# Kernel optimization log

Measured on AMD Instinct MI355X. Metric: run time of the kernel, lower is better.

Reference implementation:

```python
import jax, jax.numpy as jnp
import numpy as np

N = 50000
E = 400000
IN_DIM = 256
H1, D1 = 4, 128   # gat1: heads=4, hidden=128, concat -> 512
H2, D2 = 1, 64    # gat2: heads=1, out=64, concat=False
NEG_SLOPE = 0.2


def setup_inputs() -> dict:
    key = jax.random.key(0)
    ks = jax.random.split(key, 12)
    x = jax.random.normal(ks[0], (N, IN_DIM), dtype=jnp.float32)
    edge_index = jax.random.randint(ks[1], (2, E), 0, N, dtype=jnp.int64)
    edge_attr = jax.random.normal(ks[2], (E,), dtype=jnp.float32)
    # Glorot-ish init for weights, zeros for biases (as in PyG GATConv)
    def glorot(k, shape):
        fan = shape[0] + shape[-1]
        return jax.random.normal(k, shape, dtype=jnp.float32) * jnp.sqrt(2.0 / fan)
    W1 = glorot(ks[3], (IN_DIM, H1 * D1))
    a1_src = glorot(ks[4], (H1, D1))
    a1_dst = glorot(ks[5], (H1, D1))
    b1 = jnp.zeros((H1 * D1,), dtype=jnp.float32)
    W2 = glorot(ks[6], (H1 * D1, H2 * D2))
    a2_src = glorot(ks[7], (H2, D2))
    a2_dst = glorot(ks[8], (H2, D2))
    b2 = jnp.zeros((D2,), dtype=jnp.float32)
    return {"x": x, "edge_index": edge_index, "edge_attr": edge_attr,
            "W1": W1, "a1_src": a1_src, "a1_dst": a1_dst, "b1": b1,
            "W2": W2, "a2_src": a2_src, "a2_dst": a2_dst, "b2": b2}


def _gat_layer(x, src, dst, W, a_s, a_d, b, heads, d, concat):
    n = x.shape[0]
    h = (x @ W).reshape(n, heads, d)                      # [N,H,D]
    alpha_s = jnp.einsum('nhd,hd->nh', h, a_s)            # [N,H]
    alpha_d = jnp.einsum('nhd,hd->nh', h, a_d)
    e = jax.nn.leaky_relu(alpha_s[src] + alpha_d[dst], NEG_SLOPE)  # [Etot,H]
    # segment softmax over incoming edges of each dst node
    emax = jax.ops.segment_max(e, dst, num_segments=n)
    ex = jnp.exp(e - emax[dst])
    denom = jax.ops.segment_sum(ex, dst, num_segments=n)
    alpha = ex / (denom[dst] + 1e-16)                     # [Etot,H]
    msg = h[src] * alpha[:, :, None]                      # [Etot,H,D]
    out = jax.ops.segment_sum(msg, dst, num_segments=n)   # [N,H,D]
    out = out.reshape(n, heads * d) if concat else out.mean(axis=1)
    return out + b


def reference(x, edge_index, edge_attr, W1, a1_src, a1_dst, b1,
              W2, a2_src, a2_dst, b2):
    # edge_attr is ignored (GATConv built without edge_dim)
    loop = jnp.arange(N, dtype=edge_index.dtype)          # PyG add_self_loops=True
    src = jnp.concatenate([edge_index[0], loop])
    dst = jnp.concatenate([edge_index[1], loop])
    h = _gat_layer(x, src, dst, W1, a1_src, a1_dst, b1, H1, D1, True)
    h = jax.nn.elu(h)
    out = _gat_layer(h, src, dst, W2, a2_src, a2_dst, b2, H2, D2, False)
    return out
```

## Files before the change

### kernel.cpp

```cpp
#include <hip/hip_runtime.h>
#include <cstdint>

typedef unsigned short u16;
typedef short bf16x8_t __attribute__((ext_vector_type(8)));
typedef float f32x4_t __attribute__((ext_vector_type(4)));

#define DEVFN __device__ __forceinline__

DEVFN u16 f2bf(float f) {
  unsigned u = __builtin_bit_cast(unsigned, f);
  u = (u + 0x7fffu + ((u >> 16) & 1u)) >> 16;
  return (u16)u;
}
DEVFN float bf2f(u16 s) {
  unsigned u = ((unsigned)s) << 16;
  return __builtin_bit_cast(float, u);
}
DEVFN unsigned pk2bf(float a, float b) {
  return (unsigned)f2bf(a) | ((unsigned)f2bf(b) << 16);
}

DEVFN void gload_lds16(const u16* g, u16* l) {
  __builtin_amdgcn_global_load_lds(
      (const __attribute__((address_space(1))) void*)g,
      (__attribute__((address_space(3))) void*)l, 16, 0, 0);
}

__global__ void prep_kernel(const float* __restrict__ W1, const float* __restrict__ W2,
                            const float* __restrict__ a1s, const float* __restrict__ a1d,
                            const int* __restrict__ edst,
                            u16* __restrict__ w1t, u16* __restrict__ w2t,
                            float* __restrict__ ws1, float* __restrict__ wd1,
                            int* __restrict__ cnt, int e) {
  int b = blockIdx.x;
  if (b < 512) {
    int idx = b * 256 + threadIdx.x;
    int k = idx >> 9, m = idx & 511;
    w1t[m * 256 + k] = f2bf(W1[idx]);
  } else if (b < 640) {
    int idx = (b - 512) * 256 + threadIdx.x;
    int k = idx >> 6, m = idx & 63;
    w2t[m * 512 + k] = f2bf(W2[idx]);
  } else if (b < 648) {
    int b2 = b - 640;
    int h = b2 >> 1;
    int isD = b2 & 1;
    const float* av = (isD ? a1d : a1s) + h * 128;
    int k = threadIdx.x;
    float sum = 0.f;
#pragma unroll 8
    for (int d = 0; d < 128; ++d)
      sum = fmaf(W1[k * 512 + h * 128 + d], av[d], sum);
    (isD ? wd1 : ws1)[h * 256 + k] = sum;
  } else {
    int i = (b - 648) * 256 + threadIdx.x;
    if (i < e) atomicAdd(&cnt[edst[i]], 1);
  }
}

__global__ __launch_bounds__(256) void conv_alpha_kernel(
    const float* __restrict__ x, const float* __restrict__ ws1, const float* __restrict__ wd1,
    u16* __restrict__ xb, float* __restrict__ as1, float* __restrict__ ad1, int n)
{
  int node = (blockIdx.x * 256 + threadIdx.x) >> 6;
  int lane = threadIdx.x & 63;
  if (node >= n) return;
  float4 xv = *reinterpret_cast<const float4*>(x + (size_t)node * 256 + lane * 4);
  uint2 pk;
  pk.x = pk2bf(xv.x, xv.y);
  pk.y = pk2bf(xv.z, xv.w);
  *reinterpret_cast<uint2*>(xb + (size_t)node * 256 + lane * 4) = pk;

  float p[8];
#pragma unroll
  for (int v = 0; v < 8; ++v) {
    const float* wv = (v < 4 ? ws1 : wd1) + (v & 3) * 256 + lane * 4;
    float4 w4 = *reinterpret_cast<const float4*>(wv);
    p[v] = xv.x * w4.x + xv.y * w4.y + xv.z * w4.z + xv.w * w4.w;
  }
#pragma unroll
  for (int d = 1; d < 64; d <<= 1) {
#pragma unroll
    for (int v = 0; v < 8; ++v) p[v] += __shfl_xor(p[v], d, 64);
  }
  if (lane == 0) {
    *reinterpret_cast<float4*>(as1 + (size_t)node * 4) = make_float4(p[0], p[1], p[2], p[3]);
    *reinterpret_cast<float4*>(ad1 + (size_t)node * 4) = make_float4(p[4], p[5], p[6], p[7]);
  }
}

DEVFN int block_scan_256(int v, int tid, int* wsum) {
#pragma unroll
  for (int d = 1; d < 64; d <<= 1) {
    int u = __shfl_up(v, d, 64);
    if ((tid & 63) >= d) v += u;
  }
  if ((tid & 63) == 63) wsum[tid >> 6] = v;
  __syncthreads();
  int add = 0;
#pragma unroll
  for (int w = 0; w < 4; ++w) add += (w < (tid >> 6)) ? wsum[w] : 0;
  __syncthreads();
  return v + add;
}

__global__ __launch_bounds__(256) void scan_a_kernel(const int* __restrict__ cnt, int* __restrict__ bsum, int n) {
  __shared__ int ws4[4];
  int i = blockIdx.x * 256 + threadIdx.x;
  int v = (i < n) ? cnt[i] + 1 : 0;
  int incl = block_scan_256(v, threadIdx.x, ws4);
  if (threadIdx.x == 255) bsum[blockIdx.x] = incl;
}

__global__ __launch_bounds__(256) void scan_c_kernel(
    const int* __restrict__ cnt, const int* __restrict__ bsum,
    int* __restrict__ rowoff, int* __restrict__ cursor, int n)
{
  __shared__ int ws4[4];
  __shared__ int ws4b[4];
  __shared__ int base_sh;
  int pre = 0;
  for (int w = threadIdx.x; w < blockIdx.x; w += 256) pre += bsum[w];
#pragma unroll
  for (int d = 1; d < 64; d <<= 1) pre += __shfl_xor(pre, d, 64);
  if ((threadIdx.x & 63) == 0) ws4b[threadIdx.x >> 6] = pre;
  __syncthreads();
  if (threadIdx.x == 0) base_sh = ws4b[0] + ws4b[1] + ws4b[2] + ws4b[3];
  int i = blockIdx.x * 256 + threadIdx.x;
  int v = (i < n) ? cnt[i] + 1 : 0;
  int incl = block_scan_256(v, threadIdx.x, ws4);
  int off = base_sh + incl - v;
  if (i < n) {
    rowoff[i] = off;
    cursor[i] = off;
    if (i == n - 1) rowoff[n] = off + v;
  }
}

__global__ void scatter_kernel(const int* __restrict__ srcs, const int* __restrict__ dsts,
                               int* __restrict__ cursor, int* __restrict__ csr, int e, int n) {
  int i = blockIdx.x * 256 + threadIdx.x;
  if (i >= e + n) return;
  int s, d;
  if (i < e) { s = srcs[i]; d = dsts[i]; }
  else       { s = i - e; d = s; }
  int pos = atomicAdd(&cursor[d], 1);
  csr[pos] = s;
}

__global__ __launch_bounds__(256) void aggx_kernel(
    const u16* __restrict__ xb, const float* __restrict__ as1,
    const float* __restrict__ ad1, const int* __restrict__ rowoff,
    const int* __restrict__ csr, u16* __restrict__ aggx, size_t plane, int n)
{
  int node = (blockIdx.x * 256 + threadIdx.x) >> 6;
  int lane = threadIdx.x & 63;
  if (node >= n) return;
  int e0 = rowoff[node], e1 = rowoff[node + 1];
  float4 adv = *reinterpret_cast<const float4*>(ad1 + (size_t)node * 4);
  const unsigned dimb = (unsigned)lane * 4;

  float acc[4][4];
#pragma unroll
  for (int h = 0; h < 4; ++h)
#pragma unroll
    for (int d = 0; d < 4; ++d) acc[h][d] = 0.f;
  float den[4] = {0.f, 0.f, 0.f, 0.f};

  for (int e = e0; e < e1; ++e) {
    unsigned s = (unsigned)csr[e];
    float4 a4 = *reinterpret_cast<const float4*>(as1 + ((size_t)s << 2));
    float ex[4];
    {
      float t0 = a4.x + adv.x, t1 = a4.y + adv.y, t2 = a4.z + adv.z, t3 = a4.w + adv.w;
      ex[0] = __expf(fmaxf(t0, 0.2f * t0));
      ex[1] = __expf(fmaxf(t1, 0.2f * t1));
      ex[2] = __expf(fmaxf(t2, 0.2f * t2));
      ex[3] = __expf(fmaxf(t3, 0.2f * t3));
    }
#pragma unroll
    for (int h = 0; h < 4; ++h) den[h] += ex[h];
    uint2 xv = *reinterpret_cast<const uint2*>(xb + (((size_t)s << 8) + dimb));
    float xf[4];
    xf[0] = bf2f((u16)(xv.x & 0xffffu));
    xf[1] = bf2f((u16)(xv.x >> 16));
    xf[2] = bf2f((u16)(xv.y & 0xffffu));
    xf[3] = bf2f((u16)(xv.y >> 16));
#pragma unroll
    for (int h = 0; h < 4; ++h)
#pragma unroll
      for (int d = 0; d < 4; ++d) acc[h][d] = fmaf(ex[h], xf[d], acc[h][d]);
  }

#pragma unroll
  for (int h = 0; h < 4; ++h) {
    float inv = 1.f / (den[h] + 1e-16f);
    uint2 o;
    o.x = pk2bf(acc[h][0] * inv, acc[h][1] * inv);
    o.y = pk2bf(acc[h][2] * inv, acc[h][3] * inv);
    *reinterpret_cast<uint2*>(aggx + (size_t)h * plane + ((size_t)node << 8) + dimb) = o;
  }
}

template<int BM, int BN, int WROWS, int K, int BK, int NP>
__global__ __launch_bounds__(256) void gemm1_kernel(
    const u16* __restrict__ Aall, const u16* __restrict__ BT,
    const float* __restrict__ b1, u16* __restrict__ C, int M, size_t plane)
{
  constexpr int WM = BM / WROWS;
  constexpr int MF = WM / 16;
  constexpr int NF = BN / 16;
  constexpr int KK = BK / 32;
  static_assert(BK == 64, "swizzle derived for 128B rows");
  __shared__ __align__(16) u16 sA[BM][BK];
  __shared__ __align__(16) u16 sB[BN][BK];

  const int tid = threadIdx.x;
  const int lane = tid & 63;
  const int wr = tid >> 6;

  const int bid = blockIdx.x;
  const int xcd = bid & 7;
  const int rest = bid >> 3;
  const int p = rest & (NP - 1);
  const int rb = rest / NP;
  const int r = rb * 8 + xcd;
  const int NRB = (M + BM - 1) / BM;
  if (r >= NRB) return;
  const int brow = r * BM;
  const int bcol = p * BN;
  const u16* A = Aall + (size_t)p * plane;

  f32x4_t acc[MF][NF];
#pragma unroll
  for (int i = 0; i < MF; ++i)
#pragma unroll
    for (int j = 0; j < NF; ++j) acc[i][j] = f32x4_t{0.f, 0.f, 0.f, 0.f};

  const int rsel = lane & 15;
  const int kgrp = (lane >> 4) * 8;
  const int rx = (rsel & 7) * 8;

#pragma unroll
  for (int k0 = 0; k0 < K; k0 += BK) {
    constexpr int RA = BM * BK / 2048;
    bf16x8_t av[RA];
#pragma unroll
    for (int c = 0; c < RA; ++c) {
      int t = c * 256 + tid;
      int row = t >> 3;
      int gr = brow + row; gr = gr < M ? gr : M - 1;
      av[c] = *reinterpret_cast<const bf16x8_t*>(A + (size_t)gr * K + k0 + (t & 7) * 8);
    }
#pragma unroll
    for (int c = 0; c < RA; ++c) {
      int t = c * 256 + tid;
      int row = t >> 3;
      int slot = (t & 7) ^ (row & 7);
      *reinterpret_cast<bf16x8_t*>(&sA[0][0] + row * BK + slot * 8) = av[c];
    }
    constexpr int RB = BN * BK / 2048;
#pragma unroll
    for (int c = 0; c < RB; ++c) {
      int t = c * 256 + tid;
      int row = t >> 3;
      int col = ((t & 7) ^ (row & 7)) * 8;
      gload_lds16(BT + (size_t)(bcol + row) * K + k0 + col, &sB[0][0] + t * 8);
    }
    __syncthreads();
#pragma unroll
    for (int kk = 0; kk < KK; ++kk) {
      const int cswz = (kk * 32 + kgrp) ^ rx;
      bf16x8_t af[MF], bfr[NF];
#pragma unroll
      for (int i = 0; i < MF; ++i) {
        int row = wr * WM + i * 16 + rsel;
        af[i] = *reinterpret_cast<const bf16x8_t*>(&sA[0][0] + row * BK + cswz);
      }
#pragma unroll
      for (int j = 0; j < NF; ++j) {
        int row = j * 16 + rsel;
        bfr[j] = *reinterpret_cast<const bf16x8_t*>(&sB[0][0] + row * BK + cswz);
      }
#pragma unroll
      for (int i = 0; i < MF; ++i)
#pragma unroll
        for (int j = 0; j < NF; ++j)
          acc[i][j] = __builtin_amdgcn_mfma_f32_16x16x32_bf16(af[i], bfr[j], acc[i][j], 0, 0, 0);
    }
    __syncthreads();
  }

  const int crow0 = (lane >> 4) * 4;
  const int ccol = lane & 15;
#pragma unroll
  for (int i = 0; i < MF; ++i)
#pragma unroll
    for (int j = 0; j < NF; ++j)
#pragma unroll
      for (int rr = 0; rr < 4; ++rr) {
        int gr = brow + wr * WM + i * 16 + crow0 + rr;
        int gc = bcol + j * 16 + ccol;
        if (gr < M) {
          float v = acc[i][j][rr] + b1[gc];
          v = v > 0.f ? v : (__expf(v) - 1.0f);
          C[(size_t)gr * 512 + gc] = f2bf(v);
        }
      }
}

template<int BM, int BN, int WROWS, int K, int BK, int H, int DH>
__global__ __launch_bounds__(256) void gemm_alpha_kernel(
    const u16* __restrict__ A, const u16* __restrict__ BT, u16* __restrict__ C,
    const float* __restrict__ a_s, const float* __restrict__ a_d,
    float* __restrict__ as_out, float* __restrict__ ad_out, int M, int N)
{
  static_assert(BN == DH, "alpha store ownership");
  static_assert(BK == 64, "swizzle derived for 128B rows");
  constexpr int WM = BM / WROWS;
  constexpr int MF = WM / 16;
  constexpr int NF = BN / 16;
  constexpr int KK = BK / 32;
  __shared__ __align__(16) u16 sA[BM][BK];
  __shared__ __align__(16) u16 sB[BN][BK];

  const int tid = threadIdx.x;
  const int lane = tid & 63;
  const int wr = tid >> 6;
  const int brow = blockIdx.x * BM;
  const int bcol = blockIdx.y * BN;

  f32x4_t acc[MF][NF];
#pragma unroll
  for (int i = 0; i < MF; ++i)
#pragma unroll
    for (int j = 0; j < NF; ++j) acc[i][j] = f32x4_t{0.f, 0.f, 0.f, 0.f};

  const int rsel = lane & 15;
  const int kgrp = (lane >> 4) * 8;
  const int rx = (rsel & 7) * 8;

#pragma unroll
  for (int k0 = 0; k0 < K; k0 += BK) {
    constexpr int RA = BM * BK / 2048;
#pragma unroll
    for (int c = 0; c < RA; ++c) {
      int t = c * 256 + tid;
      int row = t >> 3;
      int col = ((t & 7) ^ (row & 7)) * 8;
      int gr = brow + row; gr = gr < M ? gr : M - 1;
      gload_lds16(A + (size_t)gr * K + k0 + col, &sA[0][0] + t * 8);
    }
    constexpr int RB = BN * BK / 2048;
#pragma unroll
    for (int c = 0; c < RB; ++c) {
      int t = c * 256 + tid;
      int row = t >> 3;
      int col = ((t & 7) ^ (row & 7)) * 8;
      gload_lds16(BT + (size_t)(bcol + row) * K + k0 + col, &sB[0][0] + t * 8);
    }
    __syncthreads();
#pragma unroll
    for (int kk = 0; kk < KK; ++kk) {
      const int cswz = (kk * 32 + kgrp) ^ rx;
      bf16x8_t af[MF], bfr[NF];
#pragma unroll
      for (int i = 0; i < MF; ++i) {
        int row = wr * WM + i * 16 + rsel;
        af[i] = *reinterpret_cast<const bf16x8_t*>(&sA[0][0] + row * BK + cswz);
      }
#pragma unroll
      for (int j = 0; j < NF; ++j) {
        int row = j * 16 + rsel;
        bfr[j] = *reinterpret_cast<const bf16x8_t*>(&sB[0][0] + row * BK + cswz);
      }
#pragma unroll
      for (int i = 0; i < MF; ++i)
#pragma unroll
        for (int j = 0; j < NF; ++j)
          acc[i][j] = __builtin_amdgcn_mfma_f32_16x16x32_bf16(af[i], bfr[j], acc[i][j], 0, 0, 0);
    }
    __syncthreads();
  }

  const int crow0 = (lane >> 4) * 4;
  const int ccol = lane & 15;

#pragma unroll
  for (int i = 0; i < MF; ++i)
#pragma unroll
    for (int j = 0; j < NF; ++j)
#pragma unroll
      for (int rr = 0; rr < 4; ++rr) {
        int gr = brow + wr * WM + i * 16 + crow0 + rr;
        int gc = bcol + j * 16 + ccol;
        if (gr < M) C[(size_t)gr * N + gc] = f2bf(acc[i][j][rr]);
      }

  const int head = bcol / DH;
  float asv[NF], adv[NF];
#pragma unroll
  for (int j = 0; j < NF; ++j) {
    int gc = bcol + j * 16 + ccol;
    asv[j] = a_s[gc];
    adv[j] = a_d[gc];
  }
#pragma unroll
  for (int i = 0; i < MF; ++i) {
#pragma unroll
    for (int rr = 0; rr < 4; ++rr) {
      float ps = 0.f, pd = 0.f;
#pragma unroll
      for (int j = 0; j < NF; ++j) {
        float v = acc[i][j][rr];
        ps = fmaf(v, asv[j], ps);
        pd = fmaf(v, adv[j], pd);
      }
#pragma unroll
      for (int d = 1; d < 16; d <<= 1) {
        ps += __shfl_xor(ps, d, 64);
        pd += __shfl_xor(pd, d, 64);
      }
      if ((lane & 15) == 0) {
        int gr = brow + wr * WM + i * 16 + crow0 + rr;
        if (gr < M) {
          as_out[(size_t)gr * H + head] = ps;
          ad_out[(size_t)gr * H + head] = pd;
        }
      }
    }
  }
}

__global__ __launch_bounds__(256) void agg2_kernel(
    const u16* __restrict__ h2, const float* __restrict__ as2,
    const float* __restrict__ ad2, const int* __restrict__ rowoff,
    const int* __restrict__ csr, const float* __restrict__ b2,
    float* __restrict__ out, int n)
{
  int node = (blockIdx.x * 256 + threadIdx.x) >> 5;
  int l32 = threadIdx.x & 31;
  if (node >= n) return;
  int e0 = rowoff[node], e1 = rowoff[node + 1];
  float advn = ad2[node];

  float acc0 = 0.f, acc1 = 0.f, den = 0.f;
  for (int e = e0; e < e1; ++e) {
    unsigned s = (unsigned)csr[e];
    float t = as2[s] + advn;
    float l = fmaxf(t, 0.2f * t);
    float ex = __expf(l);
    den += ex;
    unsigned hv = *reinterpret_cast<const unsigned*>(h2 + (s << 6) + l32 * 2);
    acc0 = fmaf(ex, bf2f((u16)(hv & 0xffffu)), acc0);
    acc1 = fmaf(ex, bf2f((u16)(hv >> 16)), acc1);
  }
  float inv = 1.f / (den + 1e-16f);
  float2 o;
  o.x = acc0 * inv + b2[l32 * 2];
  o.y = acc1 * inv + b2[l32 * 2 + 1];
  *reinterpret_cast<float2*>(out + (((size_t)node) << 6) + l32 * 2) = o;
}

extern "C" void kernel_launch(void* const* d_in, const int* in_sizes, int n_in,
                              void* d_out, int out_size, void* d_ws, size_t ws_size,
                              hipStream_t stream) {
  const float* x   = (const float*)d_in[0];
  const int*   ei  = (const int*)d_in[1];
  const float* W1  = (const float*)d_in[3];
  const float* a1s = (const float*)d_in[4];
  const float* a1d = (const float*)d_in[5];
  const float* b1  = (const float*)d_in[6];
  const float* W2  = (const float*)d_in[7];
  const float* a2s = (const float*)d_in[8];
  const float* a2d = (const float*)d_in[9];
  const float* b2  = (const float*)d_in[10];
  float* out = (float*)d_out;

  const int IN_DIM = 256, H1D1 = 512, D2 = 64;
  const int N = in_sizes[0] / IN_DIM;
  const int E = in_sizes[1] / 2;

  char* ws = (char*)d_ws;
  size_t off = 0;
  auto alloc = [&](size_t bytes) -> void* {
    void* p = ws + off;
    off += (bytes + 255) & ~(size_t)255;
    return p;
  };
  u16*  w1t    = (u16*)alloc((size_t)H1D1 * IN_DIM * 2);
  u16*  w2t    = (u16*)alloc((size_t)D2 * H1D1 * 2);
  float* ws1   = (float*)alloc(4 * 256 * 4);
  float* wd1   = (float*)alloc(4 * 256 * 4);
  u16*  xb     = (u16*)alloc((size_t)N * IN_DIM * 2);
  float* as1   = (float*)alloc((size_t)N * 4 * 4);
  float* ad1   = (float*)alloc((size_t)N * 4 * 4);
  int*  cnt    = (int*)alloc((size_t)N * 4);
  int*  cursor = (int*)alloc((size_t)N * 4);
  int*  rowoff = (int*)alloc((size_t)(N + 1) * 4);
  int*  bsum   = (int*)alloc(256 * 4);
  int*  csr    = (int*)alloc((size_t)(E + N) * 4);
  size_t plane = (size_t)N * IN_DIM;
  u16*  aggx   = (u16*)alloc(4 * plane * 2);
  u16*  h1o    = (u16*)alloc((size_t)N * H1D1 * 2);
  (void)n_in; (void)out_size; (void)ws_size;

  u16*   h2b = xb;
  float* as2 = (float*)(xb + (size_t)N * D2);
  float* ad2 = as2 + N;

  const int* esrc = ei;
  const int* edst = ei + E;

  (void)hipMemsetAsync(cnt, 0, (size_t)N * 4, stream);

  int eb = (E + 255) / 256;
  prep_kernel<<<648 + eb, 256, 0, stream>>>(W1, W2, a1s, a1d, edst, w1t, w2t, ws1, wd1, cnt, E);

  conv_alpha_kernel<<<(N + 3) / 4, 256, 0, stream>>>(x, ws1, wd1, xb, as1, ad1, N);

  int nsb = (N + 255) / 256;
  scan_a_kernel<<<nsb, 256, 0, stream>>>(cnt, bsum, N);
  scan_c_kernel<<<nsb, 256, 0, stream>>>(cnt, bsum, rowoff, cursor, N);
  scatter_kernel<<<(E + N + 255) / 256, 256, 0, stream>>>(esrc, edst, cursor, csr, E, N);

  aggx_kernel<<<(N + 3) / 4, 256, 0, stream>>>(xb, as1, ad1, rowoff, csr, aggx, plane, N);

  const int NRB = (N + 127) / 128;
  const int g1 = ((NRB + 7) / 8) * 8 * 4;
  gemm1_kernel<128, 128, 4, 256, 64, 4><<<g1, 256, 0, stream>>>(aggx, w1t, b1, h1o, N, plane);

  dim3 g2((N + 63) / 64, 1);
  gemm_alpha_kernel<64, 64, 4, 512, 64, 1, 64><<<g2, 256, 0, stream>>>(
      h1o, w2t, h2b, a2s, a2d, as2, ad2, N, D2);

  agg2_kernel<<<((size_t)N * 32 + 255) / 256, 256, 0, stream>>>(h2b, as2, ad2, rowoff, csr, b2, out, N);
}
```

Before: 255.5 us.

## Software-pipeline GEMM k-loop with register-prefetched A and double-buffered B tiles

Both GEMM kernels now prefetch the next K-slice during the MFMA work on the current one. A is loaded into registers and B goes into a second LDS buffer. The intent is to hide global-load latency behind compute instead of stalling at each barrier. gemm_alpha switches A from direct LDS loads to register staging. The change adds LDS and register pressure, and there is a possible hazard: sA is overwritten after only one barrier per step, so a write could race with the previous step's reads.

```diff
diff --git a/kernel.cpp b/kernel.cpp
--- a/kernel.cpp
+++ b/kernel.cpp
@@ -211,9 +211,10 @@
   constexpr int MF = WM / 16;
   constexpr int NF = BN / 16;
   constexpr int KK = BK / 32;
+  constexpr int NSTEP = K / BK;
   static_assert(BK == 64, "swizzle derived for 128B rows");
   __shared__ __align__(16) u16 sA[BM][BK];
-  __shared__ __align__(16) u16 sB[BN][BK];
+  __shared__ __align__(16) u16 sB[2][BN][BK];
 
   const int tid = threadIdx.x;
   const int lane = tid & 63;
@@ -241,17 +242,27 @@
   const int kgrp = (lane >> 4) * 8;
   const int rx = (rsel & 7) * 8;
 
-#pragma unroll
-  for (int k0 = 0; k0 < K; k0 += BK) {
-    constexpr int RA = BM * BK / 2048;
-    bf16x8_t av[RA];
-#pragma unroll
-    for (int c = 0; c < RA; ++c) {
-      int t = c * 256 + tid;
-      int row = t >> 3;
-      int gr = brow + row; gr = gr < M ? gr : M - 1;
-      av[c] = *reinterpret_cast<const bf16x8_t*>(A + (size_t)gr * K + k0 + (t & 7) * 8);
-    }
+  constexpr int RA = BM * BK / 2048;
+  constexpr int RBn = BN * BK / 2048;
+  bf16x8_t av[RA];
+
+#pragma unroll
+  for (int c = 0; c < RA; ++c) {
+    int t = c * 256 + tid;
+    int row = t >> 3;
+    int gr = brow + row; gr = gr < M ? gr : M - 1;
+    av[c] = *reinterpret_cast<const bf16x8_t*>(A + (size_t)gr * K + (t & 7) * 8);
+  }
+#pragma unroll
+  for (int c = 0; c < RBn; ++c) {
+    int t = c * 256 + tid;
+    int row = t >> 3;
+    int col = ((t & 7) ^ (row & 7)) * 8;
+    gload_lds16(BT + (size_t)(bcol + row) * K + col, &sB[0][0][0] + t * 8);
+  }
+
+#pragma unroll
+  for (int k = 0; k < NSTEP; ++k) {
 #pragma unroll
     for (int c = 0; c < RA; ++c) {
       int t = c * 256 + tid;
@@ -259,15 +270,24 @@
       int slot = (t & 7) ^ (row & 7);
       *reinterpret_cast<bf16x8_t*>(&sA[0][0] + row * BK + slot * 8) = av[c];
     }
-    constexpr int RB = BN * BK / 2048;
-#pragma unroll
-    for (int c = 0; c < RB; ++c) {
-      int t = c * 256 + tid;
-      int row = t >> 3;
-      int col = ((t & 7) ^ (row & 7)) * 8;
-      gload_lds16(BT + (size_t)(bcol + row) * K + k0 + col, &sB[0][0] + t * 8);
-    }
     __syncthreads();
+    if (k + 1 < NSTEP) {
+      const int k0n = (k + 1) * BK;
+#pragma unroll
+      for (int c = 0; c < RA; ++c) {
+        int t = c * 256 + tid;
+        int row = t >> 3;
+        int gr = brow + row; gr = gr < M ? gr : M - 1;
+        av[c] = *reinterpret_cast<const bf16x8_t*>(A + (size_t)gr * K + k0n + (t & 7) * 8);
+      }
+#pragma unroll
+      for (int c = 0; c < RBn; ++c) {
+        int t = c * 256 + tid;
+        int row = t >> 3;
+        int col = ((t & 7) ^ (row & 7)) * 8;
+        gload_lds16(BT + (size_t)(bcol + row) * K + k0n + col, &sB[(k + 1) & 1][0][0] + t * 8);
+      }
+    }
 #pragma unroll
     for (int kk = 0; kk < KK; ++kk) {
       const int cswz = (kk * 32 + kgrp) ^ rx;
@@ -280,7 +300,7 @@
 #pragma unroll
       for (int j = 0; j < NF; ++j) {
         int row = j * 16 + rsel;
-        bfr[j] = *reinterpret_cast<const bf16x8_t*>(&sB[0][0] + row * BK + cswz);
+        bfr[j] = *reinterpret_cast<const bf16x8_t*>(&sB[k & 1][0][0] + row * BK + cswz);
       }
 #pragma unroll
       for (int i = 0; i < MF; ++i)
@@ -321,8 +341,9 @@
   constexpr int MF = WM / 16;
   constexpr int NF = BN / 16;
   constexpr int KK = BK / 32;
+  constexpr int NSTEP = K / BK;
   __shared__ __align__(16) u16 sA[BM][BK];
-  __shared__ __align__(16) u16 sB[BN][BK];
+  __shared__ __align__(16) u16 sB[2][BN][BK];
 
   const int tid = threadIdx.x;
   const int lane = tid & 63;
@@ -340,26 +361,52 @@
   const int kgrp = (lane >> 4) * 8;
   const int rx = (rsel & 7) * 8;
 
-#pragma unroll
-  for (int k0 = 0; k0 < K; k0 += BK) {
-    constexpr int RA = BM * BK / 2048;
+  constexpr int RA = BM * BK / 2048;
+  constexpr int RBn = BN * BK / 2048;
+  bf16x8_t av[RA];
+
+#pragma unroll
+  for (int c = 0; c < RA; ++c) {
+    int t = c * 256 + tid;
+    int row = t >> 3;
+    int gr = brow + row; gr = gr < M ? gr : M - 1;
+    av[c] = *reinterpret_cast<const bf16x8_t*>(A + (size_t)gr * K + (t & 7) * 8);
+  }
+#pragma unroll
+  for (int c = 0; c < RBn; ++c) {
+    int t = c * 256 + tid;
+    int row = t >> 3;
+    int col = ((t & 7) ^ (row & 7)) * 8;
+    gload_lds16(BT + (size_t)(bcol + row) * K + col, &sB[0][0][0] + t * 8);
+  }
+
+#pragma unroll
+  for (int k = 0; k < NSTEP; ++k) {
 #pragma unroll
     for (int c = 0; c < RA; ++c) {
       int t = c * 256 + tid;
       int row = t >> 3;
-      int col = ((t & 7) ^ (row & 7)) * 8;
-      int gr = brow + row; gr = gr < M ? gr : M - 1;
-      gload_lds16(A + (size_t)gr * K + k0 + col, &sA[0][0] + t * 8);
-    }
-    constexpr int RB = BN * BK / 2048;
-#pragma unroll
-    for (int c = 0; c < RB; ++c) {
-      int t = c * 256 + tid;
-      int row = t >> 3;
-      int col = ((t & 7) ^ (row & 7)) * 8;
-      gload_lds16(BT + (size_t)(bcol + row) * K + k0 + col, &sB[0][0] + t * 8);
+      int slot = (t & 7) ^ (row & 7);
+      *reinterpret_cast<bf16x8_t*>(&sA[0][0] + row * BK + slot * 8) = av[c];
     }
     __syncthreads();
+    if (k + 1 < NSTEP) {
+      const int k0n = (k + 1) * BK;
+#pragma unroll
+      for (int c = 0; c < RA; ++c) {
+        int t = c * 256 + tid;
+        int row = t >> 3;
+        int gr = brow + row; gr = gr < M ? gr : M - 1;
+        av[c] = *reinterpret_cast<const bf16x8_t*>(A + (size_t)gr * K + k0n + (t & 7) * 8);
+      }
+#pragma unroll
+      for (int c = 0; c < RBn; ++c) {
+        int t = c * 256 + tid;
+        int row = t >> 3;
+        int col = ((t & 7) ^ (row & 7)) * 8;
+        gload_lds16(BT + (size_t)(bcol + row) * K + k0n + col, &sB[(k + 1) & 1][0][0] + t * 8);
+      }
+    }
 #pragma unroll
     for (int kk = 0; kk < KK; ++kk) {
       const int cswz = (kk * 32 + kgrp) ^ rx;
@@ -372,7 +419,7 @@
 #pragma unroll
       for (int j = 0; j < NF; ++j) {
         int row = j * 16 + rsel;
-        bfr[j] = *reinterpret_cast<const bf16x8_t*>(&sB[0][0] + row * BK + cswz);
+        bfr[j] = *reinterpret_cast<const bf16x8_t*>(&sB[k & 1][0][0] + row * BK + cswz);
       }
 #pragma unroll
       for (int i = 0; i < MF; ++i)
```

New measurement: 267.7 us. 1.05x slower.
